# Performance work log

Hardware: AMD Instinct MI355X
Metric: run time of the kernel (lower is better)

## Reference

```python
import jax, jax.numpy as jnp
import numpy as np

L, B, E, H = 2048, 2, 1024, 16
HD = E // H


def setup_inputs() -> dict:
    key = jax.random.key(0)
    ks = jax.random.split(key, 7)
    return {
        "query": jax.random.normal(ks[0], (L, B, E), dtype=jnp.float32),
        "key": jax.random.normal(ks[1], (L, B, E), dtype=jnp.float32),
        "value": jax.random.normal(ks[2], (L, B, E), dtype=jnp.float32),
        "in_proj_weight": jax.random.normal(ks[3], (3 * E, E), dtype=jnp.float32) * 0.02,
        "in_proj_bias": jax.random.normal(ks[4], (3 * E,), dtype=jnp.float32) * 0.02,
        "out_proj_weight": jax.random.normal(ks[5], (E, E), dtype=jnp.float32) * 0.02,
        "out_proj_bias": jax.random.normal(ks[6], (E,), dtype=jnp.float32) * 0.02,
    }


def reference(query, key, value, in_proj_weight, in_proj_bias, out_proj_weight, out_proj_bias):
    l, b, e = query.shape
    scaling = jnp.asarray(HD, query.dtype) ** -0.5
    wq, wk, wv = jnp.split(in_proj_weight, 3, axis=0)
    bq, bk, bv = jnp.split(in_proj_bias, 3)
    q = (query @ wq.T + bq) * scaling          # [L,B,E]
    k = key @ wk.T + bk
    v = value @ wv.T + bv

    def to_heads(t):  # [L,B,E] -> [B*H, L, HD]
        return t.reshape(l, b * H, HD).transpose(1, 0, 2)

    q, k, v = to_heads(q), to_heads(k), to_heads(v)
    scores = jnp.einsum('nld,nmd->nlm', q, k)  # [B*H, L, L] materialized as in legacy MHA
    attn = jax.nn.softmax(scores, axis=-1)
    out = jnp.einsum('nlm,nmd->nld', attn, v)  # [B*H, L, HD]
    out = out.transpose(1, 0, 2).reshape(l, b, e)
    return out @ out_proj_weight.T + out_proj_bias
```

## Files before the change

kernel.cpp:

```cpp
#include <hip/hip_runtime.h>
#include <hip/hip_bf16.h>

typedef __attribute__((ext_vector_type(8))) short short8;
typedef __attribute__((ext_vector_type(4))) float floatx4;

#define L_SEQ 2048
#define EMB   1024
#define HD    64
#define QSCALE 0.18033688011112042f
#define FIXMAX2 11.541560327111707f

__device__ __forceinline__ unsigned short f2bf(float f) {
    unsigned int u = __float_as_uint(f);
    u += 0x7fffu + ((u >> 16) & 1u);
    return (unsigned short)(u >> 16);
}
__device__ __forceinline__ unsigned pkbf(float a, float b) {
    return (unsigned)f2bf(a) | ((unsigned)f2bf(b) << 16);
}
__device__ __forceinline__ unsigned pkbf2(float a, float b) {
    __hip_bfloat162 h = __float22bfloat162_rn(make_float2(a, b));
    unsigned u; __builtin_memcpy(&u, &h, 4); return u;
}
__device__ __forceinline__ void gld_lds16(const void* g, void* l) {
    __builtin_amdgcn_global_load_lds(
        (const __attribute__((address_space(1))) unsigned*)g,
        (__attribute__((address_space(3))) unsigned*)l, 16, 0, 0);
}
__device__ __forceinline__ float fexp2(float x) {
    return __builtin_amdgcn_exp2f(x);
}

__global__ __launch_bounds__(256) void convert_all(
    const float* __restrict__ q, const float* __restrict__ k,
    const float* __restrict__ v, const float* __restrict__ ipw,
    const float* __restrict__ opw,
    unsigned short* __restrict__ Abq, unsigned short* __restrict__ Abk,
    unsigned short* __restrict__ Abv, unsigned short* __restrict__ Wipb,
    unsigned short* __restrict__ Wopb)
{
    const int NA = 1048576, NIP = 786432;
    int idx = blockIdx.x * 256 + threadIdx.x;
    const float* src; unsigned short* dst; int o;
    if (idx < NA)            { src = q;   dst = Abq;  o = idx; }
    else if (idx < 2 * NA)   { src = k;   dst = Abk;  o = idx - NA; }
    else if (idx < 3 * NA)   { src = v;   dst = Abv;  o = idx - 2 * NA; }
    else if (idx < 3 * NA + NIP) { src = ipw; dst = Wipb; o = idx - 3 * NA; }
    else                     { src = opw; dst = Wopb; o = idx - 3 * NA - NIP; }
    float4 f = ((const float4*)src)[o];
    ((uint2*)dst)[o] = make_uint2(pkbf(f.x, f.y), pkbf(f.z, f.w));
}

__global__ __launch_bounds__(256, 3) void qkv_gemm(
    const unsigned short* __restrict__ Abq, const unsigned short* __restrict__ Abk,
    const unsigned short* __restrict__ Abv, const unsigned short* __restrict__ Wb,
    const float* __restrict__ Bip,
    unsigned short* __restrict__ Qh, unsigned short* __restrict__ Kh,
    unsigned short* __restrict__ Vt)
{
    __shared__ unsigned short lds[17408];
    unsigned short* As = lds;
    unsigned short* Bs = lds + 8192;

    const int tid = threadIdx.x, lane = tid & 63, w = tid >> 6;
    const int wm = (w & 1) * 64, wn = (w >> 1) * 64;
    const int m0 = blockIdx.x * 128, n0 = blockIdx.y * 128;
    const int cn = lane & 15, g = lane >> 4;
    const int z = n0 >> 10;
    const unsigned short* Ag = (z == 0) ? Abq : (z == 1) ? Abk : Abv;

    floatx4 acc[4][4];
    #pragma unroll
    for (int i = 0; i < 4; ++i)
        #pragma unroll
        for (int j = 0; j < 4; ++j) acc[i][j] = (floatx4){0.f, 0.f, 0.f, 0.f};

    for (int k0 = 0; k0 < EMB; k0 += 64) {
        __syncthreads();
        #pragma unroll
        for (int p = 0; p < 4; ++p) {
            int u0 = (p * 4 + w) * 64, u = u0 + lane, row = u >> 3, sl = u & 7;
            gld_lds16(Ag + (size_t)(m0 + row) * EMB + k0 + ((sl ^ (row & 7)) * 8), &As[u0 * 8]);
            gld_lds16(Wb + (size_t)(n0 + row) * EMB + k0 + ((sl ^ (row & 7)) * 8), &Bs[u0 * 8]);
        }
        __syncthreads();
        #pragma unroll
        for (int kc = 0; kc < 2; ++kc) {
            short8 a4[4], b4[4];
            #pragma unroll
            for (int i = 0; i < 4; ++i)
                a4[i] = *(const short8*)&As[(wm + i * 16 + cn) * 64 + (((kc * 4 + g) ^ (cn & 7)) * 8)];
            #pragma unroll
            for (int j = 0; j < 4; ++j)
                b4[j] = *(const short8*)&Bs[(wn + j * 16 + cn) * 64 + (((kc * 4 + g) ^ (cn & 7)) * 8)];
            #pragma unroll
            for (int i = 0; i < 4; ++i)
                #pragma unroll
                for (int j = 0; j < 4; ++j)
                    acc[i][j] = __builtin_amdgcn_mfma_f32_16x16x32_bf16(a4[i], b4[j], acc[i][j], 0, 0, 0);
        }
    }

    if (z < 2) {
        #pragma unroll
        for (int j = 0; j < 4; ++j) {
            int col = n0 + wn + j * 16 + cn;
            float bv = Bip[col];
            int o = col & 1023, h = o >> 6, d = o & 63;
            #pragma unroll
            for (int i = 0; i < 4; ++i)
                #pragma unroll
                for (int r = 0; r < 4; ++r) {
                    int rr = m0 + wm + i * 16 + g * 4 + r;
                    float vv = acc[i][j][r] + bv;
                    int l = rr >> 1, bb = rr & 1, nn = bb * 16 + h;
                    if (z == 0) Qh[((size_t)nn * L_SEQ + l) * HD + d] = f2bf(vv * QSCALE);
                    else        Kh[((size_t)nn * L_SEQ + l) * HD + d] = f2bf(vv);
                }
        }
    } else {
        __syncthreads();
        #pragma unroll
        for (int j = 0; j < 4; ++j) {
            int col_l = wn + j * 16 + cn;
            float bv = Bip[n0 + col_l];
            #pragma unroll
            for (int i = 0; i < 4; ++i) {
                int rrb = wm + i * 16 + g * 4;
                int l0 = rrb >> 1;
                float v0 = acc[i][j][0] + bv, v1 = acc[i][j][1] + bv;
                float v2 = acc[i][j][2] + bv, v3 = acc[i][j][3] + bv;
                *(unsigned*)&lds[col_l * 136 +      l0] = pkbf(v0, v2);
                *(unsigned*)&lds[col_l * 136 + 64 + l0] = pkbf(v1, v3);
            }
        }
        __syncthreads();
        int cl = tid >> 1, bb = tid & 1;
        int o = (n0 - 2048) + cl, h = o >> 6, d = o & 63;
        int nn = bb * 16 + h;
        unsigned short* dst = Vt + ((size_t)nn * HD + d) * L_SEQ + (m0 >> 1);
        const unsigned short* srcp = &lds[cl * 136 + bb * 64];
        #pragma unroll
        for (int i = 0; i < 8; ++i)
            *(uint4*)(dst + i * 8) = *(const uint4*)(srcp + i * 8);
    }
}

__global__ __launch_bounds__(256) void repack_kv(
    const unsigned short* __restrict__ Kh, const unsigned short* __restrict__ Vt,
    unsigned short* __restrict__ Kf, unsigned short* __restrict__ Vf)
{
    int Wv = blockIdx.x * 4 + (threadIdx.x >> 6);
    int lane = threadIdx.x & 63, cn = lane & 15, g = lane >> 4;
    if (Wv < 8192) {
        int n = Wv >> 8, kt = (Wv >> 1) & 127, kc = Wv & 1;
        short8 val = *(const short8*)(Kh + ((size_t)(n * 2048 + kt * 16 + cn) * 64) + kc * 32 + g * 8);
        *(short8*)(Kf + (size_t)Wv * 512 + lane * 8) = val;
    } else {
        int cv = Wv - 8192;
        int n = cv >> 8, dt = (cv >> 6) & 3, K32 = cv & 63;
        short8 val = *(const short8*)(Vt + ((size_t)(n * 64 + dt * 16 + cn) * 2048) + K32 * 32 + g * 8);
        *(short8*)(Vf + (size_t)cv * 512 + lane * 8) = val;
    }
}

__global__ __launch_bounds__(256, 2) void flash_attn_k(
    const unsigned short* __restrict__ Qh, const unsigned short* __restrict__ Kf,
    const unsigned short* __restrict__ Vf, unsigned short* __restrict__ Oh)
{
    const int id = blockIdx.y * 32 + blockIdx.x;
    const int xcd = id & 7, slot = id >> 3;
    const int n = xcd * 4 + (slot & 3);
    const int q0 = (slot >> 2) * 64;

    __shared__ float Uf[2 * 64 * 41];
    unsigned short* Ps = (unsigned short*)Uf;

    const int tid = threadIdx.x, lane = tid & 63, w = tid >> 6;
    const int qh = w & 1, kh = w >> 1;
    const int cn = lane & 15, g = lane >> 4;

    short8 ones;
    #pragma unroll
    for (int j = 0; j < 8; ++j) ones[j] = (short)0x3F80;

    short8 qf[2][2];
    #pragma unroll
    for (int i = 0; i < 2; ++i)
        #pragma unroll
        for (int kc = 0; kc < 2; ++kc)
            qf[i][kc] = *(const short8*)(Qh + ((size_t)n * L_SEQ + q0 + qh * 32 + i * 16 + cn) * HD + kc * 32 + g * 8);

    floatx4 acc_o[2][4], acc_l[2];
    #pragma unroll
    for (int i = 0; i < 2; ++i) {
        acc_l[i] = (floatx4){0.f, 0.f, 0.f, 0.f};
        #pragma unroll
        for (int d = 0; d < 4; ++d) acc_o[i][d] = (floatx4){0.f, 0.f, 0.f, 0.f};
    }

    const unsigned short* Kbase = Kf + (size_t)n * 131072;
    const unsigned short* Vbase = Vf + (size_t)n * 131072;

    for (int t = kh * 16; t < kh * 16 + 16; ++t) {
        short8 kf[2][4], vf[4][2];
        #pragma unroll
        for (int kc = 0; kc < 2; ++kc)
            #pragma unroll
            for (int j = 0; j < 4; ++j)
                kf[kc][j] = *(const short8*)(Kbase + (size_t)(((t * 4 + j) * 2 + kc) * 512) + lane * 8);
        #pragma unroll
        for (int d = 0; d < 4; ++d)
            #pragma unroll
            for (int kc = 0; kc < 2; ++kc)
                vf[d][kc] = *(const short8*)(Vbase + (size_t)((d * 64 + t * 2 + kc) * 512) + lane * 8);

        floatx4 s[2][4];
        #pragma unroll
        for (int i = 0; i < 2; ++i)
            #pragma unroll
            for (int j = 0; j < 4; ++j) s[i][j] = (floatx4){0.f, 0.f, 0.f, 0.f};
        __builtin_amdgcn_s_setprio(1);
        #pragma unroll
        for (int kc = 0; kc < 2; ++kc)
            #pragma unroll
            for (int i = 0; i < 2; ++i)
                #pragma unroll
                for (int j = 0; j < 4; ++j)
                    s[i][j] = __builtin_amdgcn_mfma_f32_16x16x32_bf16(kf[kc][j], qf[i][kc], s[i][j], 0, 0, 0);
        __builtin_amdgcn_s_setprio(0);

        #pragma unroll
        for (int i = 0; i < 2; ++i)
            #pragma unroll
            for (int j = 0; j < 4; ++j) {
                float p0 = fexp2(s[i][j][0] - FIXMAX2);
                float p1 = fexp2(s[i][j][1] - FIXMAX2);
                float p2 = fexp2(s[i][j][2] - FIXMAX2);
                float p3 = fexp2(s[i][j][3] - FIXMAX2);
                *(uint2*)&Ps[(w * 32 + i * 16 + cn) * 72 + j * 16 + g * 4] =
                    make_uint2(pkbf2(p0, p1), pkbf2(p2, p3));
            }

        #pragma unroll
        for (int kc = 0; kc < 2; ++kc) {
            short8 pa[2];
            #pragma unroll
            for (int i = 0; i < 2; ++i)
                pa[i] = *(const short8*)&Ps[(w * 32 + i * 16 + cn) * 72 + kc * 32 + g * 8];
            __builtin_amdgcn_s_setprio(1);
            #pragma unroll
            for (int i = 0; i < 2; ++i) {
                #pragma unroll
                for (int d = 0; d < 4; ++d)
                    acc_o[i][d] = __builtin_amdgcn_mfma_f32_16x16x32_bf16(pa[i], vf[d][kc], acc_o[i][d], 0, 0, 0);
                acc_l[i] = __builtin_amdgcn_mfma_f32_16x16x32_bf16(pa[i], ones, acc_l[i], 0, 0, 0);
            }
            __builtin_amdgcn_s_setprio(0);
        }
    }

    const int ub = qh * (64 * 41) + lane * 41;

    __syncthreads();
    if (kh) {
        #pragma unroll
        for (int i = 0; i < 2; ++i) {
            #pragma unroll
            for (int d = 0; d < 4; ++d)
                #pragma unroll
                for (int r = 0; r < 4; ++r)
                    Uf[ub + i * 20 + d * 4 + r] = acc_o[i][d][r];
            #pragma unroll
            for (int r = 0; r < 4; ++r)
                Uf[ub + i * 20 + 16 + r] = acc_l[i][r];
        }
    }
    __syncthreads();
    if (!kh) {
        #pragma unroll
        for (int i = 0; i < 2; ++i) {
            #pragma unroll
            for (int d = 0; d < 4; ++d)
                #pragma unroll
                for (int r = 0; r < 4; ++r)
                    acc_o[i][d][r] += Uf[ub + i * 20 + d * 4 + r];
            #pragma unroll
            for (int r = 0; r < 4; ++r)
                acc_l[i][r] += Uf[ub + i * 20 + 16 + r];
        }
        const int bb = n >> 4, h = n & 15;
        #pragma unroll
        for (int i = 0; i < 2; ++i)
            #pragma unroll
            for (int r = 0; r < 4; ++r) {
                float inv = 1.0f / acc_l[i][r];
                int l = q0 + qh * 32 + i * 16 + g * 4 + r;
                #pragma unroll
                for (int d = 0; d < 4; ++d) {
                    int e = h * 64 + d * 16 + cn;
                    Oh[((size_t)l * 2 + bb) * EMB + e] = f2bf(acc_o[i][d][r] * inv);
                }
            }
    }
}

__global__ __launch_bounds__(256, 3) void out_gemm(
    const unsigned short* __restrict__ Oh, const unsigned short* __restrict__ Wob,
    const float* __restrict__ bo, float* __restrict__ out)
{
    __shared__ unsigned short As[128 * 64];
    __shared__ unsigned short Bs[128 * 64];

    const int tid = threadIdx.x, lane = tid & 63, w = tid >> 6;
    const int wm = (w & 1) * 64, wn = (w >> 1) * 64;
    const int m0 = blockIdx.x * 128, n0 = blockIdx.y * 128;
    const int cn = lane & 15, g = lane >> 4;

    floatx4 acc[4][4];
    #pragma unroll
    for (int i = 0; i < 4; ++i)
        #pragma unroll
        for (int j = 0; j < 4; ++j) acc[i][j] = (floatx4){0.f, 0.f, 0.f, 0.f};

    for (int k0 = 0; k0 < EMB; k0 += 64) {
        __syncthreads();
        #pragma unroll
        for (int p = 0; p < 4; ++p) {
            int u0 = (p * 4 + w) * 64, u = u0 + lane, row = u >> 3, sl = u & 7;
            gld_lds16(Oh  + (size_t)(m0 + row) * EMB + k0 + ((sl ^ (row & 7)) * 8), &As[u0 * 8]);
            gld_lds16(Wob + (size_t)(n0 + row) * EMB + k0 + ((sl ^ (row & 7)) * 8), &Bs[u0 * 8]);
        }
        __syncthreads();
        #pragma unroll
        for (int kc = 0; kc < 2; ++kc) {
            short8 a4[4], b4[4];
            #pragma unroll
            for (int i = 0; i < 4; ++i)
                a4[i] = *(const short8*)&As[(wm + i * 16 + cn) * 64 + (((kc * 4 + g) ^ (cn & 7)) * 8)];
            #pragma unroll
            for (int j = 0; j < 4; ++j)
                b4[j] = *(const short8*)&Bs[(wn + j * 16 + cn) * 64 + (((kc * 4 + g) ^ (cn & 7)) * 8)];
            #pragma unroll
            for (int i = 0; i < 4; ++i)
                #pragma unroll
                for (int j = 0; j < 4; ++j)
                    acc[i][j] = __builtin_amdgcn_mfma_f32_16x16x32_bf16(a4[i], b4[j], acc[i][j], 0, 0, 0);
        }
    }

    #pragma unroll
    for (int j = 0; j < 4; ++j) {
        int col = n0 + wn + j * 16 + cn;
        float bv = bo[col];
        #pragma unroll
        for (int i = 0; i < 4; ++i)
            #pragma unroll
            for (int r = 0; r < 4; ++r)
                out[(size_t)(m0 + wm + i * 16 + g * 4 + r) * EMB + col] = acc[i][j][r] + bv;
    }
}

extern "C" void kernel_launch(void* const* d_in, const int* in_sizes, int n_in,
                              void* d_out, int out_size, void* d_ws, size_t ws_size,
                              hipStream_t stream) {
    const float* q   = (const float*)d_in[0];
    const float* k   = (const float*)d_in[1];
    const float* v   = (const float*)d_in[2];
    const float* ipw = (const float*)d_in[3];
    const float* ipb = (const float*)d_in[4];
    const float* opw = (const float*)d_in[5];
    const float* opb = (const float*)d_in[6];
    float* out = (float*)d_out;

    const size_t HE = (size_t)32 * L_SEQ * HD;
    unsigned short* Qh   = (unsigned short*)d_ws;
    unsigned short* Kh   = Qh + HE;
    unsigned short* Vt   = Kh + HE;
    unsigned short* Wipb = Vt + HE;
    unsigned short* Wopb = Wipb + (size_t)3 * EMB * EMB;
    unsigned short* Abq  = Wopb + (size_t)EMB * EMB;
    unsigned short* Abk  = Abq + HE;
    unsigned short* Abv  = Abk + HE;
    unsigned short* Oh   = Abq;
    unsigned short* Kf   = Abk;
    unsigned short* Vf   = Abv;

    convert_all<<<dim3(16384), 256, 0, stream>>>(q, k, v, ipw, opw, Abq, Abk, Abv, Wipb, Wopb);
    qkv_gemm<<<dim3(32, 24), 256, 0, stream>>>(Abq, Abk, Abv, Wipb, ipb, Qh, Kh, Vt);
    repack_kv<<<dim3(4096), 256, 0, stream>>>(Kh, Vt, Kf, Vf);
    flash_attn_k<<<dim3(32, 32), 256, 0, stream>>>(Qh, Kf, Vf, Oh);
    out_gemm<<<dim3(32, 8), 256, 0, stream>>>(Oh, Wopb, opb, out);
}
```

Measured before the change: 221.2 us.

## Split flash attention keys four ways per block with serial cross-wave reduction

Each wave now handles all 64 queries of the block but only a quarter of the key range (8 tiles instead of 16), so every K/V fragment loaded feeds twice as many MFMAs. K fragments are loaded per j-column and V fragments per kc chunk to keep register pressure manageable. The final merge becomes a serial three-step reduction through shared memory with extra barriers. Register usage grows with 4x4 accumulators, which may hurt occupancy under launch_bounds(256,2).

```diff
diff --git a/kernel.cpp b/kernel.cpp
--- a/kernel.cpp
+++ b/kernel.cpp
@@ -173,27 +173,26 @@
     const int n = xcd * 4 + (slot & 3);
     const int q0 = (slot >> 2) * 64;
 
-    __shared__ float Uf[2 * 64 * 41];
-    unsigned short* Ps = (unsigned short*)Uf;
+    __shared__ unsigned short Ps[4 * 64 * 72];
+    float* Uf = (float*)Ps;
 
     const int tid = threadIdx.x, lane = tid & 63, w = tid >> 6;
-    const int qh = w & 1, kh = w >> 1;
     const int cn = lane & 15, g = lane >> 4;
 
     short8 ones;
     #pragma unroll
     for (int j = 0; j < 8; ++j) ones[j] = (short)0x3F80;
 
-    short8 qf[2][2];
-    #pragma unroll
-    for (int i = 0; i < 2; ++i)
+    short8 qf[4][2];
+    #pragma unroll
+    for (int i = 0; i < 4; ++i)
         #pragma unroll
         for (int kc = 0; kc < 2; ++kc)
-            qf[i][kc] = *(const short8*)(Qh + ((size_t)n * L_SEQ + q0 + qh * 32 + i * 16 + cn) * HD + kc * 32 + g * 8);
-
-    floatx4 acc_o[2][4], acc_l[2];
-    #pragma unroll
-    for (int i = 0; i < 2; ++i) {
+            qf[i][kc] = *(const short8*)(Qh + ((size_t)n * L_SEQ + q0 + i * 16 + cn) * HD + kc * 32 + g * 8);
+
+    floatx4 acc_o[4][4], acc_l[4];
+    #pragma unroll
+    for (int i = 0; i < 4; ++i) {
         acc_l[i] = (floatx4){0.f, 0.f, 0.f, 0.f};
         #pragma unroll
         for (int d = 0; d < 4; ++d) acc_o[i][d] = (floatx4){0.f, 0.f, 0.f, 0.f};
@@ -202,70 +201,58 @@
     const unsigned short* Kbase = Kf + (size_t)n * 131072;
     const unsigned short* Vbase = Vf + (size_t)n * 131072;
 
-    for (int t = kh * 16; t < kh * 16 + 16; ++t) {
-        short8 kf[2][4], vf[4][2];
-        #pragma unroll
-        for (int kc = 0; kc < 2; ++kc)
-            #pragma unroll
-            for (int j = 0; j < 4; ++j)
-                kf[kc][j] = *(const short8*)(Kbase + (size_t)(((t * 4 + j) * 2 + kc) * 512) + lane * 8);
-        #pragma unroll
-        for (int d = 0; d < 4; ++d)
-            #pragma unroll
-            for (int kc = 0; kc < 2; ++kc)
-                vf[d][kc] = *(const short8*)(Vbase + (size_t)((d * 64 + t * 2 + kc) * 512) + lane * 8);
-
-        floatx4 s[2][4];
-        #pragma unroll
-        for (int i = 0; i < 2; ++i)
-            #pragma unroll
-            for (int j = 0; j < 4; ++j) s[i][j] = (floatx4){0.f, 0.f, 0.f, 0.f};
-        __builtin_amdgcn_s_setprio(1);
-        #pragma unroll
-        for (int kc = 0; kc < 2; ++kc)
-            #pragma unroll
-            for (int i = 0; i < 2; ++i)
-                #pragma unroll
-                for (int j = 0; j < 4; ++j)
-                    s[i][j] = __builtin_amdgcn_mfma_f32_16x16x32_bf16(kf[kc][j], qf[i][kc], s[i][j], 0, 0, 0);
-        __builtin_amdgcn_s_setprio(0);
-
-        #pragma unroll
-        for (int i = 0; i < 2; ++i)
-            #pragma unroll
-            for (int j = 0; j < 4; ++j) {
-                float p0 = fexp2(s[i][j][0] - FIXMAX2);
-                float p1 = fexp2(s[i][j][1] - FIXMAX2);
-                float p2 = fexp2(s[i][j][2] - FIXMAX2);
-                float p3 = fexp2(s[i][j][3] - FIXMAX2);
-                *(uint2*)&Ps[(w * 32 + i * 16 + cn) * 72 + j * 16 + g * 4] =
+    for (int t = w * 8; t < w * 8 + 8; ++t) {
+        #pragma unroll
+        for (int j = 0; j < 4; ++j) {
+            short8 kf0 = *(const short8*)(Kbase + (size_t)((((t * 4 + j) * 2 + 0) * 512)) + lane * 8);
+            short8 kf1 = *(const short8*)(Kbase + (size_t)((((t * 4 + j) * 2 + 1) * 512)) + lane * 8);
+            floatx4 sj[4];
+            __builtin_amdgcn_s_setprio(1);
+            #pragma unroll
+            for (int i = 0; i < 4; ++i) {
+                sj[i] = __builtin_amdgcn_mfma_f32_16x16x32_bf16(kf0, qf[i][0], (floatx4){0.f, 0.f, 0.f, 0.f}, 0, 0, 0);
+                sj[i] = __builtin_amdgcn_mfma_f32_16x16x32_bf16(kf1, qf[i][1], sj[i], 0, 0, 0);
+            }
+            __builtin_amdgcn_s_setprio(0);
+            #pragma unroll
+            for (int i = 0; i < 4; ++i) {
+                float p0 = fexp2(sj[i][0] - FIXMAX2);
+                float p1 = fexp2(sj[i][1] - FIXMAX2);
+                float p2 = fexp2(sj[i][2] - FIXMAX2);
+                float p3 = fexp2(sj[i][3] - FIXMAX2);
+                *(uint2*)&Ps[(w * 64 + i * 16 + cn) * 72 + j * 16 + g * 4] =
                     make_uint2(pkbf2(p0, p1), pkbf2(p2, p3));
             }
+        }
 
         #pragma unroll
         for (int kc = 0; kc < 2; ++kc) {
-            short8 pa[2];
-            #pragma unroll
-            for (int i = 0; i < 2; ++i)
-                pa[i] = *(const short8*)&Ps[(w * 32 + i * 16 + cn) * 72 + kc * 32 + g * 8];
+            short8 vf[4];
+            #pragma unroll
+            for (int d = 0; d < 4; ++d)
+                vf[d] = *(const short8*)(Vbase + (size_t)((d * 64 + t * 2 + kc) * 512) + lane * 8);
+            short8 pa[4];
+            #pragma unroll
+            for (int i = 0; i < 4; ++i)
+                pa[i] = *(const short8*)&Ps[(w * 64 + i * 16 + cn) * 72 + kc * 32 + g * 8];
             __builtin_amdgcn_s_setprio(1);
             #pragma unroll
-            for (int i = 0; i < 2; ++i) {
+            for (int i = 0; i < 4; ++i) {
                 #pragma unroll
                 for (int d = 0; d < 4; ++d)
-                    acc_o[i][d] = __builtin_amdgcn_mfma_f32_16x16x32_bf16(pa[i], vf[d][kc], acc_o[i][d], 0, 0, 0);
+                    acc_o[i][d] = __builtin_amdgcn_mfma_f32_16x16x32_bf16(pa[i], vf[d], acc_o[i][d], 0, 0, 0);
                 acc_l[i] = __builtin_amdgcn_mfma_f32_16x16x32_bf16(pa[i], ones, acc_l[i], 0, 0, 0);
             }
             __builtin_amdgcn_s_setprio(0);
         }
     }
 
-    const int ub = qh * (64 * 41) + lane * 41;
+    const int ub = lane * 81;
 
     __syncthreads();
-    if (kh) {
-        #pragma unroll
-        for (int i = 0; i < 2; ++i) {
+    if (w == 3) {
+        #pragma unroll
+        for (int i = 0; i < 4; ++i) {
             #pragma unroll
             for (int d = 0; d < 4; ++d)
                 #pragma unroll
@@ -277,9 +264,11 @@
         }
     }
     __syncthreads();
-    if (!kh) {
-        #pragma unroll
-        for (int i = 0; i < 2; ++i) {
+    if (w == 2 || w == 1) {
+    }
+    if (w == 2) {
+        #pragma unroll
+        for (int i = 0; i < 4; ++i) {
             #pragma unroll
             for (int d = 0; d < 4; ++d)
                 #pragma unroll
@@ -289,13 +278,63 @@
             for (int r = 0; r < 4; ++r)
                 acc_l[i][r] += Uf[ub + i * 20 + 16 + r];
         }
+        #pragma unroll
+        for (int i = 0; i < 4; ++i) {
+            #pragma unroll
+            for (int d = 0; d < 4; ++d)
+                #pragma unroll
+                for (int r = 0; r < 4; ++r)
+                    Uf[ub + i * 20 + d * 4 + r] = acc_o[i][d][r];
+            #pragma unroll
+            for (int r = 0; r < 4; ++r)
+                Uf[ub + i * 20 + 16 + r] = acc_l[i][r];
+        }
+    }
+    __syncthreads();
+    if (w == 1) {
+        #pragma unroll
+        for (int i = 0; i < 4; ++i) {
+            #pragma unroll
+            for (int d = 0; d < 4; ++d)
+                #pragma unroll
+                for (int r = 0; r < 4; ++r)
+                    acc_o[i][d][r] += Uf[ub + i * 20 + d * 4 + r];
+            #pragma unroll
+            for (int r = 0; r < 4; ++r)
+                acc_l[i][r] += Uf[ub + i * 20 + 16 + r];
+        }
+        #pragma unroll
+        for (int i = 0; i < 4; ++i) {
+            #pragma unroll
+            for (int d = 0; d < 4; ++d)
+                #pragma unroll
+                for (int r = 0; r < 4; ++r)
+                    Uf[ub + i * 20 + d * 4 + r] = acc_o[i][d][r];
+            #pragma unroll
+            for (int r = 0; r < 4; ++r)
+                Uf[ub + i * 20 + 16 + r] = acc_l[i][r];
+        }
+    }
+    __syncthreads();
+    if (w == 0) {
+        #pragma unroll
+        for (int i = 0; i < 4; ++i) {
+            #pragma unroll
+            for (int d = 0; d < 4; ++d)
+                #pragma unroll
+                for (int r = 0; r < 4; ++r)
+                    acc_o[i][d][r] += Uf[ub + i * 20 + d * 4 + r];
+            #pragma unroll
+            for (int r = 0; r < 4; ++r)
+                acc_l[i][r] += Uf[ub + i * 20 + 16 + r];
+        }
         const int bb = n >> 4, h = n & 15;
         #pragma unroll
-        for (int i = 0; i < 2; ++i)
+        for (int i = 0; i < 4; ++i)
             #pragma unroll
             for (int r = 0; r < 4; ++r) {
                 float inv = 1.0f / acc_l[i][r];
-                int l = q0 + qh * 32 + i * 16 + g * 4 + r;
+                int l = q0 + i * 16 + g * 4 + r;
                 #pragma unroll
                 for (int d = 0; d < 4; ++d) {
                     int e = h * 64 + d * 16 + cn;
```

Result: no change. 220.8 us (-0.2%).
